# Kernel optimization log

Hardware: AMD Instinct MI355X
Metric: run time of the kernel (lower is better)

The kernel has to match this reference:

```python
import jax, jax.numpy as jnp
import numpy as np
import math

B, D, NH, NS, NT = 16, 256, 512, 8, 32
NV = NS * NT          # 256 prediction variables
L, H, A = 4, 8, 64    # attention layers, heads, head dim
HA = H * A            # 512
M = 512               # mlp_dim
R = 128               # resolution
EPS = 1e-5


def setup_inputs() -> dict:
    key = jax.random.key(0)
    ks = jax.random.split(key, 32)
    s = 0.02
    inp = {
        'hist_encoded': jax.random.normal(ks[0], (B, NH, D), jnp.float32),
        'hist_true_u': jax.random.uniform(ks[1], (B, NH), jnp.float32),
        'pred_encoded': jax.random.normal(ks[2], (B, NV, D), jnp.float32),
        'pred_true_u': jax.random.uniform(ks[3], (B, NV), jnp.float32),
        # dimension shifting layer
        'ds_w': jax.random.normal(ks[4], (D, HA), jnp.float32) * s,
        'ds_b': jnp.zeros((HA,), jnp.float32),
        # per-layer, per-head key/value creators: Linear(D+1 -> A)
        'key_w': jax.random.normal(ks[5], (L, H, D + 1, A), jnp.float32) * s,
        'key_b': jnp.zeros((L, H, A), jnp.float32),
        'val_w': jax.random.normal(ks[6], (L, H, D + 1, A), jnp.float32) * s,
        'val_b': jnp.zeros((L, H, A), jnp.float32),
        # layer norms
        'ln1_g': jnp.ones((L, HA), jnp.float32),
        'ln1_b': jnp.zeros((L, HA), jnp.float32),
        'ln2_g': jnp.ones((L, HA), jnp.float32),
        'ln2_b': jnp.zeros((L, HA), jnp.float32),
        # feed-forward (mlp_layers=2): HA->M, M->M, M->HA
        'ff_w1': jax.random.normal(ks[7], (L, HA, M), jnp.float32) * s,
        'ff_b1': jnp.zeros((L, M), jnp.float32),
        'ff_w2': jax.random.normal(ks[8], (L, M, M), jnp.float32) * s,
        'ff_b2': jnp.zeros((L, M), jnp.float32),
        'ff_w3': jax.random.normal(ks[9], (L, M, HA), jnp.float32) * s,
        'ff_b3': jnp.zeros((L, HA), jnp.float32),
        # dist extractor
        'de_w': jax.random.normal(ks[10], (HA, R), jnp.float32) * s,
        'de_b': jnp.zeros((R,), jnp.float32),
        'num_series': NS,
        'num_timesteps': NT,
    }
    return inp


def _ln(x, g, b):
    m = x.mean(-1, keepdims=True)
    v = ((x - m) ** 2).mean(-1, keepdims=True)
    return g * (x - m) / jnp.sqrt(v + EPS) + b


def _forward(hist_encoded, hist_true_u, pred_encoded, pred_true_u,
             ds_w, ds_b, key_w, key_b, val_w, val_b,
             ln1_g, ln1_b, ln2_g, ln2_b,
             ff_w1, ff_b1, ff_w2, ff_b2, ff_w3, ff_b3,
             de_w, de_b):
    Bm, NVm, Dm = pred_encoded.shape
    NHm = hist_encoded.shape[1]
    Lm, Hm, _, Am = key_w.shape
    W = NHm + NVm
    # identity permutation in the source loss() -> no-op
    att = pred_encoded @ ds_w + ds_b  # [B, NV, HA]
    # key/value inputs: [hist||u ; pred||u] -> [B, W, D+1]
    ki = jnp.concatenate([
        jnp.concatenate([hist_encoded, hist_true_u[:, :, None]], axis=2),
        jnp.concatenate([pred_encoded, pred_true_u[:, :, None]], axis=2)], axis=1)
    keys = jnp.einsum('bwd,lhda->lbhwa', ki, key_w) + key_b[:, None, :, None, :]
    vals = jnp.einsum('bwd,lhda->lbhwa', ki, val_w) + val_b[:, None, :, None, :]
    # flipped-triangular mask: position w is masked iff w >= NH + v
    mask = jnp.arange(W)[None, :] >= (NHm + jnp.arange(NVm)[:, None])  # [NV, W]
    scale = Am ** (-0.5)
    for l in range(Lm):
        avh = att.reshape(Bm, NVm, Hm, Am)
        prod = jnp.einsum('bvhi,bhwi->bhvw', avh, keys[l])  # [B,H,NV,W]
        prod = jnp.where(mask, -jnp.inf, prod) * scale
        w = jax.nn.softmax(prod, axis=-1)
        a = jnp.einsum('bhvw,bhwj->bvhj', w, vals[l]).reshape(Bm, NVm, Hm * Am)
        att = _ln(att + a, ln1_g[l], ln1_b[l])
        ff = jnp.maximum(att @ ff_w1[l] + ff_b1[l], 0.0)
        ff = jnp.maximum(ff @ ff_w2[l] + ff_b2[l], 0.0)
        ff = ff @ ff_w3[l] + ff_b3[l]
        att = _ln(att + ff, ln2_g[l], ln2_b[l])
    res = de_w.shape[-1]
    target = jnp.clip(jnp.floor(pred_true_u[:, 1:] * res).astype(jnp.int32), 0, res - 1)
    logits = (att @ de_w + de_b)[:, 1:, :]
    lp = math.log(res) + jax.nn.log_softmax(logits, axis=2)
    lp = jnp.take_along_axis(lp, target[:, :, None], axis=2)[:, :, 0]
    return -lp.sum(axis=1)  # [B]


def reference(hist_encoded, hist_true_u, pred_encoded, pred_true_u,
              ds_w, ds_b, key_w, key_b, val_w, val_b,
              ln1_g, ln1_b, ln2_g, ln2_b,
              ff_w1, ff_b1, ff_w2, ff_b2, ff_w3, ff_b3,
              de_w, de_b, num_series, num_timesteps):
    assert pred_encoded.shape[1] == num_series * num_timesteps
    return _forward(hist_encoded, hist_true_u, pred_encoded, pred_true_u,
                    ds_w, ds_b, key_w, key_b, val_w, val_b,
                    ln1_g, ln1_b, ln2_g, ln2_b,
                    ff_w1, ff_b1, ff_w2, ff_b2, ff_w3, ff_b3,
                    de_w, de_b)
```

## Files before the change

kernel.cpp:

```cpp
#include <hip/hip_runtime.h>

constexpr int kB = 16, kD = 256, kNH = 512, kNV = 256, kW = 768;
constexpr int kL = 4, kH = 8, kA = 64, kHA = 512, kM = 512, kR = 128;
constexpr int kKP = 288;
constexpr int kRows = kB * kNV;

typedef __bf16 bf16x8 __attribute__((ext_vector_type(8)));
typedef __bf16 bf16x4 __attribute__((ext_vector_type(4)));
typedef float f32x4 __attribute__((ext_vector_type(4)));

__device__ inline void load_lds16(const __bf16* g, __bf16* l) {
  __builtin_amdgcn_global_load_lds(
      (const __attribute__((address_space(1))) void*)g,
      (__attribute__((address_space(3))) void*)l, 16, 0, 0);
}

constexpr int kP1 = kB * kW * kKP;
constexpr int kP2 = 4096 * kKP;
constexpr int kP3 = 12 * 512 * 512;
constexpr int kP4 = 200704;
constexpr int kP5 = 16;
constexpr int kPT = kP1 + kP2 + kP3 + kP4 + kP5;

__global__ void prep_kernel(const float* __restrict__ hist,
                            const float* __restrict__ hist_u,
                            const float* __restrict__ pred,
                            const float* __restrict__ pred_u,
                            const float* __restrict__ kw,
                            const float* __restrict__ vw,
                            const float* __restrict__ w1,
                            const float* __restrict__ w2,
                            const float* __restrict__ w3,
                            const float* __restrict__ ds_w,
                            const float* __restrict__ de_w,
                            const float* __restrict__ key_b,
                            const float* __restrict__ val_b,
                            __bf16* __restrict__ ki,
                            __bf16* __restrict__ kvwt,
                            __bf16* __restrict__ ffwt,
                            __bf16* __restrict__ ds_wt,
                            __bf16* __restrict__ de_wt,
                            float* __restrict__ kvb,
                            float* __restrict__ outz) {
  int i = blockIdx.x * 256 + threadIdx.x;
  if (i < kP1) {
    int d = i % kKP;
    int bw = i / kKP;
    int w = bw % kW;
    int b = bw / kW;
    float v = 0.f;
    if (d < 257) {
      if (w < kNH)
        v = (d < kD) ? hist[((size_t)b * kNH + w) * kD + d] : hist_u[b * kNH + w];
      else {
        int p = w - kNH;
        v = (d < kD) ? pred[((size_t)b * kNV + p) * kD + d] : pred_u[b * kNV + p];
      }
    }
    ki[i] = (__bf16)v;
  } else if (i < kP1 + kP2) {
    int j = i - kP1;
    int d = j % kKP;
    int c = j / kKP;
    float v = 0.f;
    if (d < 257) {
      bool isv = c >= 2048;
      int cc = isv ? c - 2048 : c;
      int l = cc >> 9, rest = cc & 511;
      int h = rest >> 6, a = rest & 63;
      size_t src = (((size_t)l * kH + h) * 257 + d) * kA + a;
      v = isv ? vw[src] : kw[src];
    }
    kvwt[j] = (__bf16)v;
  } else if (i < kP1 + kP2 + kP3) {
    int j = i - kP1 - kP2;
    int k = j & 511;
    int n = (j >> 9) & 511;
    int mat = j >> 18;
    int l = mat / 3, which = mat % 3;
    const float* src = which == 0 ? w1 : which == 1 ? w2 : w3;
    ffwt[j] = (__bf16)src[((size_t)l * 512 + k) * 512 + n];
  } else if (i < kP1 + kP2 + kP3 + kP4) {
    int j = i - kP1 - kP2 - kP3;
    if (j < 131072) {
      int n = j >> 8, k = j & 255;
      ds_wt[j] = (__bf16)ds_w[k * 512 + n];
    } else if (j < 196608) {
      int jj = j - 131072;
      int n = jj >> 9, k = jj & 511;
      de_wt[jj] = (__bf16)de_w[k * 128 + n];
    } else {
      int c = j - 196608;
      bool isv = c >= 2048;
      int cc = isv ? c - 2048 : c;
      int l = cc >> 9, rest = cc & 511;
      kvb[c] = isv ? val_b[l * 512 + rest] : key_b[l * 512 + rest];
    }
  } else if (i < kPT) {
    outz[i - kP1 - kP2 - kP3 - kP4] = 0.f;
  }
}

template <int BN, int OMODE, bool RELU, bool KIMAP, bool BIASROW>
__device__ __forceinline__ void gemm_core(
    int bxv, int byv, const __bf16* __restrict__ A,
    const __bf16* __restrict__ Bt, const float* __restrict__ bias,
    void* __restrict__ Cout, __bf16* __restrict__ Cout2, int K, int lda,
    int ldc, __bf16* Sm) {
  constexpr int JN = BN / 32;
  constexpr int BROWS = BN / 4;
  constexpr int SSTEP = (128 + BN) * 32;
  const int t = threadIdx.x;
  const int wid = t >> 6;
  const int lane = t & 63;
  const int bm = byv * 128;
  const int bn = bxv * BN;
  const int wm = (wid >> 1) * 64;
  const int wn = (wid & 1) * (BN / 2);
  const int sr = lane >> 2, sc = lane & 3;
  const int skey = (sr >> 1) & 3;
  const int abase = KIMAP ? ((bm >> 8) * 768 + 512 + (bm & 255)) : bm;
  const __bf16* Ag = A + (size_t)(abase + wid * 32 + sr) * lda + (sc ^ skey) * 8;
  const __bf16* Bg = Bt + (size_t)(bn + wid * BROWS + sr) * K + (sc ^ skey) * 8;
  __bf16* A0 = Sm;
  __bf16* B0 = Sm + 4096;
  __bf16* A1 = Sm + SSTEP;
  __bf16* B1 = Sm + SSTEP + 4096;

  auto stage = [&](int k0, __bf16* As, __bf16* Bs) {
    load_lds16(Ag + k0, As + (wid * 32) * 32);
    load_lds16(Ag + (size_t)16 * lda + k0, As + (wid * 32 + 16) * 32);
    load_lds16(Bg + k0, Bs + (wid * BROWS) * 32);
    if (BN == 128)
      load_lds16(Bg + (size_t)16 * K + k0, Bs + (wid * BROWS + 16) * 32);
  };

  f32x4 acc[4][JN] = {};
  const int q = lane >> 4, mr = lane & 15;
  const int rkey = (mr >> 1) & 3;
  stage(0, A0, B0);
  __syncthreads();
  for (int k0 = 0; k0 < K; k0 += 32) {
    if (k0 + 32 < K) stage(k0 + 32, A1, B1);
    bf16x8 af[4], bfr[JN];
#pragma unroll
    for (int i = 0; i < 4; ++i)
      af[i] = *(const bf16x8*)(A0 + (wm + i * 16 + mr) * 32 + (q ^ rkey) * 8);
#pragma unroll
    for (int j = 0; j < JN; ++j)
      bfr[j] = *(const bf16x8*)(B0 + (wn + j * 16 + mr) * 32 + (q ^ rkey) * 8);
#pragma unroll
    for (int i = 0; i < 4; ++i)
#pragma unroll
      for (int j = 0; j < JN; ++j)
        acc[i][j] = __builtin_amdgcn_mfma_f32_16x16x32_bf16(af[i], bfr[j],
                                                            acc[i][j], 0, 0, 0);
    __syncthreads();
    __bf16* tp = A0; A0 = A1; A1 = tp;
    tp = B0; B0 = B1; B1 = tp;
  }
  if (OMODE == 1) {
    constexpr int PS = BN + 8;
    __bf16* Cs = Sm;
#pragma unroll
    for (int j = 0; j < JN; ++j) {
      float bscol = BIASROW ? 0.f : bias[bn + wn + j * 16 + mr];
#pragma unroll
      for (int i = 0; i < 4; ++i) {
#pragma unroll
        for (int r = 0; r < 4; ++r) {
          float v = acc[i][j][r] +
                    (BIASROW ? bias[bm + wm + i * 16 + q * 4 + r] : bscol);
          if (RELU) v = fmaxf(v, 0.f);
          Cs[(wm + i * 16 + q * 4 + r) * PS + wn + j * 16 + mr] = (__bf16)v;
        }
      }
    }
    __syncthreads();
    constexpr int lpr = BN / 8;
    constexpr int rpi = 512 / BN;
    const int rl = lane / lpr, cl = (lane % lpr) * 8;
#pragma unroll
    for (int it = 0; it < BN / 16; ++it) {
      int row = wid * 32 + it * rpi + rl;
      bf16x8 v = *(const bf16x8*)&Cs[row * PS + cl];
      *(bf16x8*)((__bf16*)Cout + (size_t)(bm + row) * ldc + bn + cl) = v;
    }
  } else {
    constexpr int PSF = BN + 4;
    float* Csf = (float*)Sm;
#pragma unroll
    for (int j = 0; j < JN; ++j) {
      float bscol = bias[bn + wn + j * 16 + mr];
#pragma unroll
      for (int i = 0; i < 4; ++i) {
#pragma unroll
        for (int r = 0; r < 4; ++r) {
          float v = acc[i][j][r] + bscol;
          if (RELU) v = fmaxf(v, 0.f);
          Csf[(wm + i * 16 + q * 4 + r) * PSF + wn + j * 16 + mr] = v;
        }
      }
    }
    __syncthreads();
    const int rl = lane >> 4, cl = (lane & 15) * 4;
#pragma unroll
    for (int it = 0; it < 8; ++it) {
      int row = wid * 32 + it * 4 + rl;
      f32x4 v = *(const f32x4*)&Csf[row * PSF + cl];
      size_t gidx = (size_t)(bm + row) * ldc + bn + cl;
      *(f32x4*)((float*)Cout + gidx) = v;
      bf16x4 vb = {(__bf16)v[0], (__bf16)v[1], (__bf16)v[2], (__bf16)v[3]};
      *(bf16x4*)(Cout2 + gidx) = vb;
    }
  }
}

__global__ __launch_bounds__(256) void gemm3_kernel(
    const __bf16* __restrict__ ki, const __bf16* __restrict__ ds_wt,
    const float* __restrict__ ds_b, float* __restrict__ att,
    __bf16* __restrict__ att_bf, const __bf16* __restrict__ kv_wt,
    const float* __restrict__ kvb, __bf16* __restrict__ kvs_k,
    __bf16* __restrict__ vT) {
  __shared__ __bf16 smem[17408];
  int bid = blockIdx.x;
  if (bid < 256) {
    gemm_core<64, 2, false, true, false>(bid & 7, bid >> 3, ki, ds_wt, ds_b,
                                         att, att_bf, 256, kKP, 512, smem);
  } else if (bid < 1792) {
    int b2 = bid - 256;
    gemm_core<128, 1, false, false, false>(b2 & 15, b2 >> 4, ki, kv_wt, kvb,
                                           kvs_k, nullptr, kKP, kKP, 2048,
                                           smem);
  } else {
    int b3 = bid - 1792;
    gemm_core<128, 1, false, false, true>(b3 % 96, b3 / 96,
                                          kv_wt + (size_t)2048 * kKP, ki,
                                          kvb + 2048, vT, nullptr, kKP, kKP,
                                          12288, smem);
  }
}

template <bool RELU>
__global__ __launch_bounds__(256) void gemm_ff_kernel(
    const __bf16* __restrict__ A, const __bf16* __restrict__ Bt,
    const float* __restrict__ bias, __bf16* __restrict__ Cout) {
  __shared__ __bf16 smem[12288];
  gemm_core<64, 1, RELU, false, false>(blockIdx.x, blockIdx.y, A, Bt, bias,
                                       Cout, nullptr, 512, 512, 512, smem);
}

__global__ __launch_bounds__(256) void attn_mfma_kernel(
    const __bf16* __restrict__ attbf, const __bf16* __restrict__ kvs_k,
    const __bf16* __restrict__ vT, __bf16* __restrict__ outbf, int l) {
  const int b = blockIdx.z, h = blockIdx.y, qt = blockIdx.x;
  __shared__ __bf16 Ks[64 * 72];
  __shared__ __bf16 Vt[64 * 72];
  __shared__ __bf16 Ps[64 * 72];
  const int t = threadIdx.x;
  const int w = t >> 6, lane = t & 63;
  const int quad = lane >> 4, mr = lane & 15;
  bf16x8 aq[2];
  {
    const __bf16* qp = attbf + ((size_t)(b * kNV + qt * 64 + w * 16 + mr) * kHA +
                                h * kA + quad * 8);
    aq[0] = *(const bf16x8*)qp;
    aq[1] = *(const bf16x8*)(qp + 32);
  }
  f32x4 o[4] = {};
  float m_ = -1e30f, l_ = 0.f;
  const int cmax = kNH + qt * 64;
  const int pr = t >> 2, pc = t & 3;
  const __bf16* kbase = kvs_k + ((size_t)(b * kW + pr) * 2048 + l * 512 + h * kA);
  const __bf16* vbase = vT + (size_t)(l * 512 + h * kA + pr) * 12288 + b * kW;
  bf16x8 kc0, kc1, vc0, vc1;
  kc0 = *(const bf16x8*)(kbase + pc * 8);
  kc1 = *(const bf16x8*)(kbase + pc * 8 + 32);
  vc0 = *(const bf16x8*)(vbase + pc * 16);
  vc1 = *(const bf16x8*)(vbase + pc * 16 + 8);
  for (int c0 = 0; c0 <= cmax; c0 += 64) {
    __syncthreads();
    *(bf16x8*)&Ks[pr * 72 + pc * 8] = kc0;
    *(bf16x8*)&Ks[pr * 72 + pc * 8 + 32] = kc1;
    *(bf16x8*)&Vt[pr * 72 + pc * 16] = vc0;
    *(bf16x8*)&Vt[pr * 72 + pc * 16 + 8] = vc1;
    __syncthreads();
    if (c0 + 64 <= cmax) {
      const __bf16* kp = kbase + (size_t)(c0 + 64) * 2048;
      const __bf16* vp = vbase + c0 + 64;
      kc0 = *(const bf16x8*)(kp + pc * 8);
      kc1 = *(const bf16x8*)(kp + pc * 8 + 32);
      vc0 = *(const bf16x8*)(vp + pc * 16);
      vc1 = *(const bf16x8*)(vp + pc * 16 + 8);
    }
    f32x4 s[4];
#pragma unroll
    for (int j = 0; j < 4; ++j) {
      bf16x8 ak0 = *(const bf16x8*)&Ks[(j * 16 + mr) * 72 + quad * 8];
      bf16x8 ak1 = *(const bf16x8*)&Ks[(j * 16 + mr) * 72 + quad * 8 + 32];
      f32x4 z = {};
      z = __builtin_amdgcn_mfma_f32_16x16x32_bf16(ak0, aq[0], z, 0, 0, 0);
      z = __builtin_amdgcn_mfma_f32_16x16x32_bf16(ak1, aq[1], z, 0, 0, 0);
      s[j] = z;
    }
    const int lim = cmax - c0;
    float sv[16], mx = -1e30f;
#pragma unroll
    for (int j = 0; j < 4; ++j)
#pragma unroll
      for (int r = 0; r < 4; ++r) {
        int p = j * 16 + quad * 4 + r;
        float x = (p < lim + mr) ? s[j][r] * 0.125f : -1e30f;
        sv[j * 4 + r] = x;
        mx = fmaxf(mx, x);
      }
    mx = fmaxf(mx, __shfl_xor(mx, 16));
    mx = fmaxf(mx, __shfl_xor(mx, 32));
    float mnew = fmaxf(m_, mx);
    float corr = __expf(m_ - mnew);
    float rs = 0.f;
#pragma unroll
    for (int i = 0; i < 16; ++i) {
      sv[i] = __expf(sv[i] - mnew);
      rs += sv[i];
    }
    rs += __shfl_xor(rs, 16);
    rs += __shfl_xor(rs, 32);
    l_ = l_ * corr + rs;
    m_ = mnew;
#pragma unroll
    for (int j = 0; j < 4; ++j) {
      bf16x4 pk = {(__bf16)sv[j * 4 + 0], (__bf16)sv[j * 4 + 1],
                   (__bf16)sv[j * 4 + 2], (__bf16)sv[j * 4 + 3]};
      *(bf16x4*)&Ps[(w * 16 + mr) * 72 + j * 16 + quad * 4] = pk;
    }
#pragma unroll
    for (int r = 0; r < 4; ++r) {
      float cr = __shfl(corr, quad * 4 + r);
#pragma unroll
      for (int j = 0; j < 4; ++j) o[j][r] *= cr;
    }
    bf16x8 ap0 = *(const bf16x8*)&Ps[(w * 16 + mr) * 72 + quad * 8];
    bf16x8 ap1 = *(const bf16x8*)&Ps[(w * 16 + mr) * 72 + quad * 8 + 32];
#pragma unroll
    for (int j = 0; j < 4; ++j) {
      bf16x8 b0 = *(const bf16x8*)&Vt[(j * 16 + mr) * 72 + quad * 8];
      bf16x8 b1 = *(const bf16x8*)&Vt[(j * 16 + mr) * 72 + quad * 8 + 32];
      o[j] = __builtin_amdgcn_mfma_f32_16x16x32_bf16(ap0, b0, o[j], 0, 0, 0);
      o[j] = __builtin_amdgcn_mfma_f32_16x16x32_bf16(ap1, b1, o[j], 0, 0, 0);
    }
  }
  float invl = 1.f / l_;
#pragma unroll
  for (int r = 0; r < 4; ++r) {
    float ir = __shfl(invl, quad * 4 + r);
    int row = b * kNV + qt * 64 + w * 16 + quad * 4 + r;
#pragma unroll
    for (int j = 0; j < 4; ++j)
      outbf[(size_t)row * kHA + h * kA + j * 16 + mr] = (__bf16)(o[j][r] * ir);
  }
}

__global__ __launch_bounds__(128) void add_ln_kernel(
    float* __restrict__ att, const __bf16* __restrict__ addbf,
    const float* __restrict__ g, const float* __restrict__ be,
    __bf16* __restrict__ attbf) {
  const int row = blockIdx.x;
  const int t = threadIdx.x;
  float4* ar = (float4*)(att + (size_t)row * kHA);
  bf16x4 dv = *(const bf16x4*)(addbf + (size_t)row * kHA + t * 4);
  float4 x = ar[t];
  x.x += (float)dv[0]; x.y += (float)dv[1];
  x.z += (float)dv[2]; x.w += (float)dv[3];
  float s = x.x + x.y + x.z + x.w;
  float sq = x.x * x.x + x.y * x.y + x.z * x.z + x.w * x.w;
  for (int o = 32; o; o >>= 1) {
    s += __shfl_xor(s, o);
    sq += __shfl_xor(sq, o);
  }
  __shared__ float red[4];
  if ((t & 63) == 0) { red[(t >> 6) * 2] = s; red[(t >> 6) * 2 + 1] = sq; }
  __syncthreads();
  float S = red[0] + red[2], Q = red[1] + red[3];
  float mean = S * (1.f / kHA);
  float inv = rsqrtf(Q * (1.f / kHA) - mean * mean + 1e-5f);
  float4 gv = ((const float4*)g)[t];
  float4 bv = ((const float4*)be)[t];
  float4 y;
  y.x = gv.x * (x.x - mean) * inv + bv.x;
  y.y = gv.y * (x.y - mean) * inv + bv.y;
  y.z = gv.z * (x.z - mean) * inv + bv.z;
  y.w = gv.w * (x.w - mean) * inv + bv.w;
  ar[t] = y;
  bf16x4 yb = {(__bf16)y.x, (__bf16)y.y, (__bf16)y.z, (__bf16)y.w};
  *(bf16x4*)(attbf + (size_t)row * kHA + t * 4) = yb;
}

__global__ __launch_bounds__(256) void de_loss_kernel(
    const __bf16* __restrict__ attbf, const __bf16* __restrict__ de_wt,
    const float* __restrict__ de_b, const float* __restrict__ pred_u,
    float* __restrict__ out) {
  const int blk = blockIdx.x;
  const int t = threadIdx.x;
  const int w = t >> 6, lane = t & 63, quad = lane >> 4, mr = lane & 15;
  const int row0 = blk * 64 + w * 16;
  f32x4 acc[8] = {};
  const __bf16* Ap = attbf + (size_t)(row0 + mr) * kHA + quad * 8;
#pragma unroll 4
  for (int k0 = 0; k0 < 512; k0 += 32) {
    bf16x8 a = *(const bf16x8*)(Ap + k0);
#pragma unroll
    for (int j = 0; j < 8; ++j) {
      bf16x8 bb =
          *(const bf16x8*)(de_wt + (size_t)(j * 16 + mr) * 512 + k0 + quad * 8);
      acc[j] = __builtin_amdgcn_mfma_f32_16x16x32_bf16(a, bb, acc[j], 0, 0, 0);
    }
  }
  float dbv[8];
#pragma unroll
  for (int j = 0; j < 8; ++j) dbv[j] = de_b[j * 16 + mr];
  float lpacc = 0.f;
#pragma unroll
  for (int r = 0; r < 4; ++r) {
    int row = row0 + quad * 4 + r;
    int v = row & 255;
    float lg[8], mx = -1e30f;
#pragma unroll
    for (int j = 0; j < 8; ++j) {
      lg[j] = acc[j][r] + dbv[j];
      mx = fmaxf(mx, lg[j]);
    }
    mx = fmaxf(mx, __shfl_xor(mx, 1));
    mx = fmaxf(mx, __shfl_xor(mx, 2));
    mx = fmaxf(mx, __shfl_xor(mx, 4));
    mx = fmaxf(mx, __shfl_xor(mx, 8));
    float se = 0.f;
#pragma unroll
    for (int j = 0; j < 8; ++j) se += __expf(lg[j] - mx);
    se += __shfl_xor(se, 1);
    se += __shfl_xor(se, 2);
    se += __shfl_xor(se, 4);
    se += __shfl_xor(se, 8);
    float lse = mx + __logf(se);
    float u = pred_u[(row >> 8) * 256 + v];
    int tgt = (int)floorf(u * 128.f);
    tgt = max(0, min(127, tgt));
    float cand = (mr == (tgt & 15)) ? lg[tgt >> 4] : 0.f;
    cand += __shfl_xor(cand, 1);
    cand += __shfl_xor(cand, 2);
    cand += __shfl_xor(cand, 4);
    cand += __shfl_xor(cand, 8);
    float lp = (v >= 1) ? (4.8520302639196171f + cand - lse) : 0.f;
    lpacc += lp;
  }
  lpacc += __shfl_xor(lpacc, 16);
  lpacc += __shfl_xor(lpacc, 32);
  __shared__ float red[4];
  if (lane == 0) red[w] = lpacc;
  __syncthreads();
  if (t == 0)
    atomicAdd(&out[blk >> 2], -(red[0] + red[1] + red[2] + red[3]));
}

extern "C" void kernel_launch(void* const* d_in, const int* in_sizes, int n_in,
                              void* d_out, int out_size, void* d_ws, size_t ws_size,
                              hipStream_t stream) {
  const float* hist   = (const float*)d_in[0];
  const float* hist_u = (const float*)d_in[1];
  const float* pred   = (const float*)d_in[2];
  const float* pred_u = (const float*)d_in[3];
  const float* ds_w   = (const float*)d_in[4];
  const float* ds_b   = (const float*)d_in[5];
  const float* key_w  = (const float*)d_in[6];
  const float* key_b  = (const float*)d_in[7];
  const float* val_w  = (const float*)d_in[8];
  const float* val_b  = (const float*)d_in[9];
  const float* ln1_g  = (const float*)d_in[10];
  const float* ln1_b  = (const float*)d_in[11];
  const float* ln2_g  = (const float*)d_in[12];
  const float* ln2_b  = (const float*)d_in[13];
  const float* ff_w1  = (const float*)d_in[14];
  const float* ff_b1  = (const float*)d_in[15];
  const float* ff_w2  = (const float*)d_in[16];
  const float* ff_b2  = (const float*)d_in[17];
  const float* ff_w3  = (const float*)d_in[18];
  const float* ff_b3  = (const float*)d_in[19];
  const float* de_w   = (const float*)d_in[20];
  const float* de_b   = (const float*)d_in[21];
  float* out = (float*)d_out;

  char* ws = (char*)d_ws;
  size_t off = 0;
  auto alloc = [&](size_t bytes) { char* p = ws + off; off += bytes; return p; };
  __bf16* ki_bf  = (__bf16*)alloc((size_t)kB * kW * kKP * 2);
  __bf16* kv_wt  = (__bf16*)alloc((size_t)4096 * kKP * 2);
  __bf16* ffw_t  = (__bf16*)alloc((size_t)12 * 512 * 512 * 2);
  __bf16* ds_wt  = (__bf16*)alloc((size_t)512 * 256 * 2);
  __bf16* de_wt  = (__bf16*)alloc((size_t)128 * 512 * 2);
  float*  kvb    = (float*)alloc((size_t)4096 * 4);
  __bf16* kvs_k  = (__bf16*)alloc((size_t)kB * kW * 2048 * 2);
  __bf16* vT     = (__bf16*)alloc((size_t)2048 * 12288 * 2);
  float*  att    = (float*)alloc((size_t)kRows * kHA * 4);
  __bf16* att_bf = (__bf16*)alloc((size_t)kRows * kHA * 2);
  __bf16* tmp_bf = (__bf16*)alloc((size_t)kRows * kHA * 2);
  __bf16* ff1_bf = (__bf16*)alloc((size_t)kRows * kM * 2);
  __bf16* ff2_bf = (__bf16*)alloc((size_t)kRows * kM * 2);

  prep_kernel<<<(kPT + 255) / 256, 256, 0, stream>>>(
      hist, hist_u, pred, pred_u, key_w, val_w, ff_w1, ff_w2, ff_w3, ds_w, de_w,
      key_b, val_b, ki_bf, kv_wt, ffw_t, ds_wt, de_wt, kvb, out);

  gemm3_kernel<<<3328, 256, 0, stream>>>(ki_bf, ds_wt, ds_b, att, att_bf, kv_wt,
                                         kvb, kvs_k, vT);

  for (int l = 0; l < kL; ++l) {
    attn_mfma_kernel<<<dim3(kNV / 64, kH, kB), 256, 0, stream>>>(
        att_bf, kvs_k, vT, tmp_bf, l);
    add_ln_kernel<<<kRows, 128, 0, stream>>>(att, tmp_bf, ln1_g + l * kHA,
                                             ln1_b + l * kHA, att_bf);
    gemm_ff_kernel<true><<<dim3(kM / 64, kRows / 128), 256, 0, stream>>>(
        att_bf, ffw_t + (size_t)(l * 3) * 262144, ff_b1 + l * kM, ff1_bf);
    gemm_ff_kernel<true><<<dim3(kM / 64, kRows / 128), 256, 0, stream>>>(
        ff1_bf, ffw_t + (size_t)(l * 3 + 1) * 262144, ff_b2 + l * kM, ff2_bf);
    gemm_ff_kernel<false><<<dim3(kHA / 64, kRows / 128), 256, 0, stream>>>(
        ff2_bf, ffw_t + (size_t)(l * 3 + 2) * 262144, ff_b3 + l * kHA, tmp_bf);
    add_ln_kernel<<<kRows, 128, 0, stream>>>(att, tmp_bf, ln2_g + l * kHA,
                                             ln2_b + l * kHA, att_bf);
  }
  de_loss_kernel<<<64, 256, 0, stream>>>(att_bf, de_wt, de_b, pred_u, out);
}
```

Measured before the change: 454.4 us.

## Fuse second residual LayerNorm into FF3 epilogue stats and downstream consumers

Removes the separate add+LayerNorm kernel after the feed-forward block. The last FF GEMM's epilogue now accumulates per-row sum and sum-of-squares of the residual via atomics, and the LN is reconstructed on the fly in the next layer's attention query load, the next add_ln kernel, and the final distribution-extractor kernel. This saves one launch and one full pass over the activations per layer. In exchange it adds atomics, extra fp32 residual reads in several consumers, and a one-pass variance formula that is less numerically robust.

```diff
diff --git a/kernel.cpp b/kernel.cpp
--- a/kernel.cpp
+++ b/kernel.cpp
@@ -20,7 +20,9 @@
 constexpr int kP3 = 12 * 512 * 512;
 constexpr int kP4 = 200704;
 constexpr int kP5 = 16;
-constexpr int kPT = kP1 + kP2 + kP3 + kP4 + kP5;
+constexpr int kP6 = kL * kRows * 2;
+constexpr int kPT0 = kP1 + kP2 + kP3 + kP4 + kP5;
+constexpr int kPT = kPT0 + kP6;
 
 __global__ void prep_kernel(const float* __restrict__ hist,
                             const float* __restrict__ hist_u,
@@ -41,7 +43,8 @@
                             __bf16* __restrict__ ds_wt,
                             __bf16* __restrict__ de_wt,
                             float* __restrict__ kvb,
-                            float* __restrict__ outz) {
+                            float* __restrict__ outz,
+                            float* __restrict__ statsz) {
   int i = blockIdx.x * 256 + threadIdx.x;
   if (i < kP1) {
     int d = i % kKP;
@@ -96,17 +99,21 @@
       int l = cc >> 9, rest = cc & 511;
       kvb[c] = isv ? val_b[l * 512 + rest] : key_b[l * 512 + rest];
     }
+  } else if (i < kPT0) {
+    outz[i - kP1 - kP2 - kP3 - kP4] = 0.f;
   } else if (i < kPT) {
-    outz[i - kP1 - kP2 - kP3 - kP4] = 0.f;
-  }
-}
-
-template <int BN, int OMODE, bool RELU, bool KIMAP, bool BIASROW>
+    statsz[i - kPT0] = 0.f;
+  }
+}
+
+template <int BN, int OMODE, bool RELU, bool KIMAP, bool BIASROW,
+          bool STATS = false>
 __device__ __forceinline__ void gemm_core(
     int bxv, int byv, const __bf16* __restrict__ A,
     const __bf16* __restrict__ Bt, const float* __restrict__ bias,
     void* __restrict__ Cout, __bf16* __restrict__ Cout2, int K, int lda,
-    int ldc, __bf16* Sm) {
+    int ldc, __bf16* Sm, const float* __restrict__ attres = nullptr,
+    float* __restrict__ stats = nullptr) {
   constexpr int JN = BN / 32;
   constexpr int BROWS = BN / 4;
   constexpr int SSTEP = (128 + BN) * 32;
@@ -158,6 +165,40 @@
     __syncthreads();
     __bf16* tp = A0; A0 = A1; A1 = tp;
     tp = B0; B0 = B1; B1 = tp;
+  }
+  if constexpr (STATS) {
+    float rs_[4][4] = {}, rq_[4][4] = {};
+#pragma unroll
+    for (int j = 0; j < JN; ++j) {
+      float bscol = bias[bn + wn + j * 16 + mr];
+#pragma unroll
+      for (int i = 0; i < 4; ++i) {
+#pragma unroll
+        for (int r = 0; r < 4; ++r) {
+          int row = bm + wm + i * 16 + q * 4 + r;
+          int col = bn + wn + j * 16 + mr;
+          float x2 = acc[i][j][r] + bscol + attres[(size_t)row * ldc + col];
+          rs_[i][r] += x2;
+          rq_[i][r] += x2 * x2;
+        }
+      }
+    }
+#pragma unroll
+    for (int i = 0; i < 4; ++i)
+#pragma unroll
+      for (int r = 0; r < 4; ++r) {
+        float s = rs_[i][r], qq = rq_[i][r];
+#pragma unroll
+        for (int o = 1; o < 16; o <<= 1) {
+          s += __shfl_xor(s, o);
+          qq += __shfl_xor(qq, o);
+        }
+        if (mr == 0) {
+          int row = bm + wm + i * 16 + q * 4 + r;
+          atomicAdd(&stats[row * 2], s);
+          atomicAdd(&stats[row * 2 + 1], qq);
+        }
+      }
   }
   if (OMODE == 1) {
     constexpr int PS = BN + 8;
@@ -241,18 +282,23 @@
   }
 }
 
-template <bool RELU>
+template <bool RELU, bool STATS>
 __global__ __launch_bounds__(256) void gemm_ff_kernel(
     const __bf16* __restrict__ A, const __bf16* __restrict__ Bt,
-    const float* __restrict__ bias, __bf16* __restrict__ Cout) {
+    const float* __restrict__ bias, __bf16* __restrict__ Cout,
+    const float* __restrict__ attres, float* __restrict__ stats) {
   __shared__ __bf16 smem[12288];
-  gemm_core<64, 1, RELU, false, false>(blockIdx.x, blockIdx.y, A, Bt, bias,
-                                       Cout, nullptr, 512, 512, 512, smem);
+  gemm_core<64, 1, RELU, false, false, STATS>(blockIdx.x, blockIdx.y, A, Bt,
+                                              bias, Cout, nullptr, 512, 512,
+                                              512, smem, attres, stats);
 }
 
 __global__ __launch_bounds__(256) void attn_mfma_kernel(
     const __bf16* __restrict__ attbf, const __bf16* __restrict__ kvs_k,
-    const __bf16* __restrict__ vT, __bf16* __restrict__ outbf, int l) {
+    const __bf16* __restrict__ vT, __bf16* __restrict__ outbf, int l,
+    const float* __restrict__ yres, const __bf16* __restrict__ fprev,
+    const float* __restrict__ stats, const float* __restrict__ g2,
+    const float* __restrict__ b2, int recon) {
   const int b = blockIdx.z, h = blockIdx.y, qt = blockIdx.x;
   __shared__ __bf16 Ks[64 * 72];
   __shared__ __bf16 Vt[64 * 72];
@@ -262,10 +308,37 @@
   const int quad = lane >> 4, mr = lane & 15;
   bf16x8 aq[2];
   {
-    const __bf16* qp = attbf + ((size_t)(b * kNV + qt * 64 + w * 16 + mr) * kHA +
-                                h * kA + quad * 8);
-    aq[0] = *(const bf16x8*)qp;
-    aq[1] = *(const bf16x8*)(qp + 32);
+    const int grow = b * kNV + qt * 64 + w * 16 + mr;
+    const size_t base = (size_t)grow * kHA + h * kA + quad * 8;
+    if (recon) {
+      const float mean = stats[grow * 2] * (1.f / kHA);
+      const float inv =
+          rsqrtf(stats[grow * 2 + 1] * (1.f / kHA) - mean * mean + 1e-5f);
+#pragma unroll
+      for (int c = 0; c < 2; ++c) {
+        const size_t o8 = base + c * 32;
+        const int cc = h * kA + quad * 8 + c * 32;
+        float4 y0 = *(const float4*)(yres + o8);
+        float4 y1 = *(const float4*)(yres + o8 + 4);
+        bf16x8 fv = *(const bf16x8*)(fprev + o8);
+        float4 ga = *(const float4*)(g2 + cc);
+        float4 gb = *(const float4*)(g2 + cc + 4);
+        float4 ba = *(const float4*)(b2 + cc);
+        float4 bb = *(const float4*)(b2 + cc + 4);
+        aq[c] = bf16x8{
+            (__bf16)(ga.x * ((y0.x + (float)fv[0]) - mean) * inv + ba.x),
+            (__bf16)(ga.y * ((y0.y + (float)fv[1]) - mean) * inv + ba.y),
+            (__bf16)(ga.z * ((y0.z + (float)fv[2]) - mean) * inv + ba.z),
+            (__bf16)(ga.w * ((y0.w + (float)fv[3]) - mean) * inv + ba.w),
+            (__bf16)(gb.x * ((y1.x + (float)fv[4]) - mean) * inv + bb.x),
+            (__bf16)(gb.y * ((y1.y + (float)fv[5]) - mean) * inv + bb.y),
+            (__bf16)(gb.z * ((y1.z + (float)fv[6]) - mean) * inv + bb.z),
+            (__bf16)(gb.w * ((y1.w + (float)fv[7]) - mean) * inv + bb.w)};
+      }
+    } else {
+      aq[0] = *(const bf16x8*)(attbf + base);
+      aq[1] = *(const bf16x8*)(attbf + base + 32);
+    }
   }
   f32x4 o[4] = {};
   float m_ = -1e30f, l_ = 0.f;
@@ -363,13 +436,27 @@
 
 __global__ __launch_bounds__(128) void add_ln_kernel(
     float* __restrict__ att, const __bf16* __restrict__ addbf,
+    const __bf16* __restrict__ fprev, const float* __restrict__ stats,
+    const float* __restrict__ g2, const float* __restrict__ b2,
     const float* __restrict__ g, const float* __restrict__ be,
-    __bf16* __restrict__ attbf) {
+    __bf16* __restrict__ attbf, int recon) {
   const int row = blockIdx.x;
   const int t = threadIdx.x;
   float4* ar = (float4*)(att + (size_t)row * kHA);
   bf16x4 dv = *(const bf16x4*)(addbf + (size_t)row * kHA + t * 4);
   float4 x = ar[t];
+  if (recon) {
+    bf16x4 fv = *(const bf16x4*)(fprev + (size_t)row * kHA + t * 4);
+    const float mean2 = stats[row * 2] * (1.f / kHA);
+    const float inv2 =
+        rsqrtf(stats[row * 2 + 1] * (1.f / kHA) - mean2 * mean2 + 1e-5f);
+    float4 g2v = ((const float4*)g2)[t];
+    float4 b2v = ((const float4*)b2)[t];
+    x.x = g2v.x * ((x.x + (float)fv[0]) - mean2) * inv2 + b2v.x;
+    x.y = g2v.y * ((x.y + (float)fv[1]) - mean2) * inv2 + b2v.y;
+    x.z = g2v.z * ((x.z + (float)fv[2]) - mean2) * inv2 + b2v.z;
+    x.w = g2v.w * ((x.w + (float)fv[3]) - mean2) * inv2 + b2v.w;
+  }
   x.x += (float)dv[0]; x.y += (float)dv[1];
   x.z += (float)dv[2]; x.w += (float)dv[3];
   float s = x.x + x.y + x.z + x.w;
@@ -397,7 +484,9 @@
 }
 
 __global__ __launch_bounds__(256) void de_loss_kernel(
-    const __bf16* __restrict__ attbf, const __bf16* __restrict__ de_wt,
+    const float* __restrict__ yres, const __bf16* __restrict__ fprev,
+    const float* __restrict__ stats, const float* __restrict__ g2,
+    const float* __restrict__ b2, const __bf16* __restrict__ de_wt,
     const float* __restrict__ de_b, const float* __restrict__ pred_u,
     float* __restrict__ out) {
   const int blk = blockIdx.x;
@@ -405,15 +494,36 @@
   const int w = t >> 6, lane = t & 63, quad = lane >> 4, mr = lane & 15;
   const int row0 = blk * 64 + w * 16;
   f32x4 acc[8] = {};
-  const __bf16* Ap = attbf + (size_t)(row0 + mr) * kHA + quad * 8;
+  const int arow = row0 + mr;
+  const float mean = stats[arow * 2] * (1.f / kHA);
+  const float inv =
+      rsqrtf(stats[arow * 2 + 1] * (1.f / kHA) - mean * mean + 1e-5f);
+  const float* Ay = yres + (size_t)arow * kHA + quad * 8;
+  const __bf16* Af = fprev + (size_t)arow * kHA + quad * 8;
 #pragma unroll 4
   for (int k0 = 0; k0 < 512; k0 += 32) {
-    bf16x8 a = *(const bf16x8*)(Ap + k0);
+    const int cc = quad * 8 + k0;
+    float4 y0 = *(const float4*)(Ay + k0);
+    float4 y1 = *(const float4*)(Ay + k0 + 4);
+    bf16x8 fv = *(const bf16x8*)(Af + k0);
+    float4 ga = *(const float4*)(g2 + cc);
+    float4 gb = *(const float4*)(g2 + cc + 4);
+    float4 ba = *(const float4*)(b2 + cc);
+    float4 bb = *(const float4*)(b2 + cc + 4);
+    bf16x8 a = {
+        (__bf16)(ga.x * ((y0.x + (float)fv[0]) - mean) * inv + ba.x),
+        (__bf16)(ga.y * ((y0.y + (float)fv[1]) - mean) * inv + ba.y),
+        (__bf16)(ga.z * ((y0.z + (float)fv[2]) - mean) * inv + ba.z),
+        (__bf16)(ga.w * ((y0.w + (float)fv[3]) - mean) * inv + ba.w),
+        (__bf16)(gb.x * ((y1.x + (float)fv[4]) - mean) * inv + bb.x),
+        (__bf16)(gb.y * ((y1.y + (float)fv[5]) - mean) * inv + bb.y),
+        (__bf16)(gb.z * ((y1.z + (float)fv[6]) - mean) * inv + bb.z),
+        (__bf16)(gb.w * ((y1.w + (float)fv[7]) - mean) * inv + bb.w)};
 #pragma unroll
     for (int j = 0; j < 8; ++j) {
-      bf16x8 bb =
+      bf16x8 bb2 =
           *(const bf16x8*)(de_wt + (size_t)(j * 16 + mr) * 512 + k0 + quad * 8);
-      acc[j] = __builtin_amdgcn_mfma_f32_16x16x32_bf16(a, bb, acc[j], 0, 0, 0);
+      acc[j] = __builtin_amdgcn_mfma_f32_16x16x32_bf16(a, bb2, acc[j], 0, 0, 0);
     }
   }
   float dbv[8];
@@ -503,29 +613,38 @@
   float*  att    = (float*)alloc((size_t)kRows * kHA * 4);
   __bf16* att_bf = (__bf16*)alloc((size_t)kRows * kHA * 2);
   __bf16* tmp_bf = (__bf16*)alloc((size_t)kRows * kHA * 2);
+  __bf16* atmp_bf= (__bf16*)alloc((size_t)kRows * kHA * 2);
   __bf16* ff1_bf = (__bf16*)alloc((size_t)kRows * kM * 2);
   __bf16* ff2_bf = (__bf16*)alloc((size_t)kRows * kM * 2);
+  float*  stats2 = (float*)alloc((size_t)kL * kRows * 2 * 4);
 
   prep_kernel<<<(kPT + 255) / 256, 256, 0, stream>>>(
       hist, hist_u, pred, pred_u, key_w, val_w, ff_w1, ff_w2, ff_w3, ds_w, de_w,
-      key_b, val_b, ki_bf, kv_wt, ffw_t, ds_wt, de_wt, kvb, out);
+      key_b, val_b, ki_bf, kv_wt, ffw_t, ds_wt, de_wt, kvb, out, stats2);
 
   gemm3_kernel<<<3328, 256, 0, stream>>>(ki_bf, ds_wt, ds_b, att, att_bf, kv_wt,
                                          kvb, kvs_k, vT);
 
   for (int l = 0; l < kL; ++l) {
+    const float* stp = stats2 + (size_t)(l > 0 ? l - 1 : 0) * kRows * 2;
+    const float* g2p = ln2_g + (l > 0 ? l - 1 : 0) * kHA;
+    const float* b2p = ln2_b + (l > 0 ? l - 1 : 0) * kHA;
     attn_mfma_kernel<<<dim3(kNV / 64, kH, kB), 256, 0, stream>>>(
-        att_bf, kvs_k, vT, tmp_bf, l);
-    add_ln_kernel<<<kRows, 128, 0, stream>>>(att, tmp_bf, ln1_g + l * kHA,
-                                             ln1_b + l * kHA, att_bf);
-    gemm_ff_kernel<true><<<dim3(kM / 64, kRows / 128), 256, 0, stream>>>(
-        att_bf, ffw_t + (size_t)(l * 3) * 262144, ff_b1 + l * kM, ff1_bf);
-    gemm_ff_kernel<true><<<dim3(kM / 64, kRows / 128), 256, 0, stream>>>(
-        ff1_bf, ffw_t + (size_t)(l * 3 + 1) * 262144, ff_b2 + l * kM, ff2_bf);
-    gemm_ff_kernel<false><<<dim3(kHA / 64, kRows / 128), 256, 0, stream>>>(
-        ff2_bf, ffw_t + (size_t)(l * 3 + 2) * 262144, ff_b3 + l * kHA, tmp_bf);
-    add_ln_kernel<<<kRows, 128, 0, stream>>>(att, tmp_bf, ln2_g + l * kHA,
-                                             ln2_b + l * kHA, att_bf);
-  }
-  de_loss_kernel<<<64, 256, 0, stream>>>(att_bf, de_wt, de_b, pred_u, out);
-}
+        att_bf, kvs_k, vT, atmp_bf, l, att, tmp_bf, stp, g2p, b2p, l > 0);
+    add_ln_kernel<<<kRows, 128, 0, stream>>>(
+        att, atmp_bf, tmp_bf, stp, g2p, b2p, ln1_g + l * kHA, ln1_b + l * kHA,
+        att_bf, l > 0);
+    gemm_ff_kernel<true, false><<<dim3(kM / 64, kRows / 128), 256, 0, stream>>>(
+        att_bf, ffw_t + (size_t)(l * 3) * 262144, ff_b1 + l * kM, ff1_bf,
+        nullptr, nullptr);
+    gemm_ff_kernel<true, false><<<dim3(kM / 64, kRows / 128), 256, 0, stream>>>(
+        ff1_bf, ffw_t + (size_t)(l * 3 + 1) * 262144, ff_b2 + l * kM, ff2_bf,
+        nullptr, nullptr);
+    gemm_ff_kernel<false, true><<<dim3(kHA / 64, kRows / 128), 256, 0, stream>>>(
+        ff2_bf, ffw_t + (size_t)(l * 3 + 2) * 262144, ff_b3 + l * kHA, tmp_bf,
+        att, stats2 + (size_t)l * kRows * 2);
+  }
+  de_loss_kernel<<<64, 256, 0, stream>>>(
+      att, tmp_bf, stats2 + (size_t)3 * kRows * 2, ln2_g + 3 * kHA,
+      ln2_b + 3 * kHA, de_wt, de_b, pred_u, out);
+}
```

Result: slower. 464.2 us (+2.2%).
